# Kernel tuning notes

Measured on AMD Instinct MI355X. Metric: run time of the kernel, lower is better.

Reference implementation:

```python
import jax, jax.numpy as jnp
import numpy as np

B, S, E = 2, 2048, 2048
NQ, NKV, HD = 16, 4, 128
WINDOW = 512
ROPE_BASE = 10000.0


def _rope(x):
    # x: [B, H, S, HD], interleaved even/odd rotation
    half = HD // 2
    freqs = 1.0 / (ROPE_BASE ** (2.0 * jnp.arange(half, dtype=jnp.float32) / HD))
    pos = jnp.arange(x.shape[2], dtype=jnp.float32)
    ang = pos[:, None] * freqs[None, :]            # [S, HD/2]
    cos = jnp.cos(ang)[None, None].astype(x.dtype)  # [1,1,S,HD/2]
    sin = jnp.sin(ang)[None, None].astype(x.dtype)
    xe = x[..., 0::2]
    xo = x[..., 1::2]
    re = xe * cos - xo * sin
    ro = xe * sin + xo * cos
    return jnp.stack([re, ro], axis=-1).reshape(x.shape)


def setup_inputs() -> dict:
    key = jax.random.key(0)
    ks = jax.random.split(key, 9)
    s_in = 1.0 / np.sqrt(E)
    s_out = 1.0 / np.sqrt(NQ * HD)
    return {
        "x": jax.random.normal(ks[0], (B, S, E), jnp.float32),
        "Wq": jax.random.normal(ks[1], (E, NQ * HD), jnp.float32) * s_in,
        "bq": jax.random.normal(ks[2], (NQ * HD,), jnp.float32) * 0.01,
        "Wk": jax.random.normal(ks[3], (E, NKV * HD), jnp.float32) * s_in,
        "bk": jax.random.normal(ks[4], (NKV * HD,), jnp.float32) * 0.01,
        "Wv": jax.random.normal(ks[5], (E, NKV * HD), jnp.float32) * s_in,
        "bv": jax.random.normal(ks[6], (NKV * HD,), jnp.float32) * 0.01,
        "Wo": jax.random.normal(ks[7], (NQ * HD, E), jnp.float32) * s_out,
        "bo": jax.random.normal(ks[8], (E,), jnp.float32) * 0.01,
    }


def reference(x, Wq, bq, Wk, bk, Wv, bv, Wo, bo):
    b, s, _ = x.shape
    q = (x @ Wq + bq).reshape(b, s, NQ, HD).transpose(0, 2, 1, 3)   # [B,NQ,S,HD]
    k = (x @ Wk + bk).reshape(b, s, NKV, HD).transpose(0, 2, 1, 3)  # [B,NKV,S,HD]
    v = (x @ Wv + bv).reshape(b, s, NKV, HD).transpose(0, 2, 1, 3)
    q = _rope(q)
    k = _rope(k)
    rep = NQ // NKV
    k = jnp.repeat(k, rep, axis=1)  # [B,NQ,S,HD], matches torch repeat pattern
    v = jnp.repeat(v, rep, axis=1)
    scores = jnp.einsum("bhqd,bhkd->bhqk", q, k) / np.sqrt(HD)
    i = jnp.arange(s)[:, None]
    j = jnp.arange(s)[None, :]
    allowed = (j <= i) & ((i - j) <= WINDOW)  # sliding-window causal mask
    scores = jnp.where(allowed[None, None], scores, -jnp.inf)
    weights = jax.nn.softmax(scores, axis=-1)
    out = jnp.einsum("bhqk,bhkd->bhqd", weights, v)
    out = out.transpose(0, 2, 1, 3).reshape(b, s, NQ * HD)
    return out @ Wo + bo
```

## Files before the change

kernel.cpp:

```cpp
#include <hip/hip_runtime.h>
#include <hip/hip_bf16.h>
#include <math.h>

#define BB 2
#define SS 2048
#define EE 2048
#define NQ 16
#define NKV 4
#define HD 128
#define WINDOW 512

typedef __hip_bfloat16 bf16;
typedef short short8 __attribute__((ext_vector_type(8)));
typedef float f32x4 __attribute__((ext_vector_type(4)));

__device__ __forceinline__ float toF(bf16 v) { return __bfloat162float(v); }
__device__ __forceinline__ bf16 toB(float v) { return __float2bfloat16(v); }

__device__ __forceinline__ void gld_lds16(const void* g, void* l) {
    __builtin_amdgcn_global_load_lds(
        (const __attribute__((address_space(1))) void*)g,
        (__attribute__((address_space(3))) void*)l, 16, 0, 0);
}

template <int V> __device__ __forceinline__ void waitvm() {
    if constexpr (V == 8)      asm volatile("s_waitcnt vmcnt(8)" ::: "memory");
    else if constexpr (V == 6) asm volatile("s_waitcnt vmcnt(6)" ::: "memory");
    else if constexpr (V == 5) asm volatile("s_waitcnt vmcnt(5)" ::: "memory");
    else if constexpr (V == 4) asm volatile("s_waitcnt vmcnt(4)" ::: "memory");
    else if constexpr (V == 3) asm volatile("s_waitcnt vmcnt(3)" ::: "memory");
    else                       asm volatile("s_waitcnt vmcnt(0)" ::: "memory");
}
__device__ __forceinline__ void waitlgkm0() {
    asm volatile("s_waitcnt lgkmcnt(0)" ::: "memory");
}

__global__ __launch_bounds__(256) void convert_bf16(const float* __restrict__ in,
                                                    bf16* __restrict__ out, int n) {
    int i = (blockIdx.x * 256 + threadIdx.x) * 4;
    if (i >= n) return;
    const float4 v = *(const float4*)(in + i);
    bf16 o[4] = {toB(v.x), toB(v.y), toB(v.z), toB(v.w)};
    *(uint2*)(out + i) = *(const uint2*)o;
}

__global__ __launch_bounds__(256) void convert_transpose(const float* __restrict__ in,
                                                         bf16* __restrict__ out,
                                                         int K, int N) {
    __shared__ float tile[32][33];
    const int t = threadIdx.x;
    const int tx = t & 31, ty = t >> 5;
    const int n0 = blockIdx.x * 32, k0 = blockIdx.y * 32;
#pragma unroll
    for (int r = 0; r < 4; r++)
        tile[ty + r * 8][tx] = in[(size_t)(k0 + ty + r * 8) * N + n0 + tx];
    __syncthreads();
#pragma unroll
    for (int r = 0; r < 4; r++)
        out[(size_t)(n0 + ty + r * 8) * K + k0 + tx] = toB(tile[tx][ty + r * 8]);
}

__global__ __launch_bounds__(256) void convert_transpose_qkv(
    const float* __restrict__ Wq, const float* __restrict__ Wk,
    const float* __restrict__ Wv, bf16* __restrict__ out) {
    __shared__ float tile[32][33];
    const int t = threadIdx.x;
    const int tx = t & 31, ty = t >> 5;
    const int n0 = blockIdx.x * 32, k0 = blockIdx.y * 32;
    const float* src; int N, nl0;
    if (n0 < 2048)      { src = Wq; N = 2048; nl0 = n0; }
    else if (n0 < 2560) { src = Wk; N = 512;  nl0 = n0 - 2048; }
    else                { src = Wv; N = 512;  nl0 = n0 - 2560; }
#pragma unroll
    for (int r = 0; r < 4; r++)
        tile[ty + r * 8][tx] = src[(size_t)(k0 + ty + r * 8) * N + nl0 + tx];
    __syncthreads();
#pragma unroll
    for (int r = 0; r < 4; r++)
        out[(size_t)(n0 + ty + r * 8) * 2048 + k0 + tx] = toB(tile[tx][ty + r * 8]);
}

template <int MODE, int BM, int BN>
__global__ __launch_bounds__(512, 2) void mfma_gemm_v6(
    const bf16* __restrict__ A, const bf16* __restrict__ BT,
    const float* __restrict__ b0, const float* __restrict__ b1,
    const float* __restrict__ b2,
    float* __restrict__ Yf,
    bf16* __restrict__ Yq, bf16* __restrict__ Yk, bf16* __restrict__ Yv,
    int M, int N, int K) {
    constexpr int NI = BM / 2 / 16;
    constexpr int NJ = BN / 4 / 16;
    constexpr int LA = BM / 64;
    constexpr int LB = BN / 64;
    constexpr int SL = LA + LB;

    __shared__ __align__(16) bf16 As[3][BM * 64];
    __shared__ __align__(16) bf16 Bs[3][BN * 64];

    const int tid = threadIdx.x;
    const int lane = tid & 63;
    const int w = tid >> 6;
    const int wm = w >> 2;
    const int wn = w & 3;

    const int gx = gridDim.x, gy = gridDim.y;
    const int lin = blockIdx.y * gx + blockIdx.x;
    const int xcd = lin & 7;
    const int idx = lin >> 3;
    const int rpx = gy >> 3;
    const int tn = idx / rpx;
    const int tm = xcd * rpx + (idx % rpx);
    const int m0 = tm * BM, n0 = tn * BN;

    const int lr = lane & 15;
    const int lq = lane >> 4;
    const int NT = K >> 6;

    const int srow = tid >> 3;
    const int sslot = tid & 7;

    auto stage = [&](int s) {
        bf16* Ad = &As[s % 3][0];
#pragma unroll
        for (int l = 0; l < LA; l++) {
            const int row = l * 64 + srow;
            const int g = sslot ^ (row & 7);
            gld_lds16(A + (size_t)(m0 + row) * K + s * 64 + g * 8,
                      Ad + l * 4096 + w * 512);
        }
        bf16* Bd = &Bs[s % 3][0];
#pragma unroll
        for (int l = 0; l < LB; l++) {
            const int row = l * 64 + srow;
            const int g = sslot ^ (row & 7);
            gld_lds16(BT + (size_t)(n0 + row) * K + s * 64 + g * 8,
                      Bd + l * 4096 + w * 512);
        }
    };

    auto readf = [&](int s, int kk, short8 (&fA)[NI], short8 (&fB)[NJ]) {
        const bf16* Asl = &As[s % 3][0];
        const bf16* Bsl = &Bs[s % 3][0];
#pragma unroll
        for (int i = 0; i < NI; i++) {
            const int row = wm * (NI * 16) + i * 16 + lr;
            const int sl = ((kk << 2) | lq) ^ (row & 7);
            fA[i] = *(const short8*)(Asl + row * 64 + sl * 8);
        }
#pragma unroll
        for (int j = 0; j < NJ; j++) {
            const int row = wn * (NJ * 16) + j * 16 + lr;
            const int sl = ((kk << 2) | lq) ^ (row & 7);
            fB[j] = *(const short8*)(Bsl + row * 64 + sl * 8);
        }
    };

    f32x4 acc[NI][NJ];
#pragma unroll
    for (int i = 0; i < NI; i++)
#pragma unroll
        for (int j = 0; j < NJ; j++) acc[i][j] = (f32x4)0.f;

    auto cluster = [&](short8 (&fA)[NI], short8 (&fB)[NJ]) {
        __builtin_amdgcn_s_setprio(1);
#pragma unroll
        for (int i = 0; i < NI; i++)
#pragma unroll
            for (int j = 0; j < NJ; j++)
                acc[i][j] = __builtin_amdgcn_mfma_f32_16x16x32_bf16(fA[i], fB[j],
                                                                    acc[i][j], 0, 0, 0);
        __builtin_amdgcn_s_setprio(0);
    };

    stage(0); stage(1);
    waitvm<SL>();
    __builtin_amdgcn_s_barrier();
    __builtin_amdgcn_sched_barrier(0);
    short8 fA0[NI], fB0[NJ], fA1[NI], fB1[NJ];
    readf(0, 0, fA0, fB0);

    for (int t = 0; t < NT; ++t) {
        if (t + 2 < NT) stage(t + 2);
        readf(t, 1, fA1, fB1);
        cluster(fA0, fB0);
        waitlgkm0();
        if (t + 2 < NT) waitvm<SL>(); else waitvm<0>();
        __builtin_amdgcn_s_barrier();
        __builtin_amdgcn_sched_barrier(0);
        if (t + 1 < NT) readf(t + 1, 0, fA0, fB0);
        cluster(fA1, fB1);
    }

    if (MODE == 0) {
#pragma unroll
        for (int j = 0; j < NJ; j++) {
            const int col = n0 + wn * (NJ * 16) + j * 16 + lr;
            const float bj = b0[col];
#pragma unroll
            for (int i = 0; i < NI; i++) {
                const int row = m0 + wm * (NI * 16) + i * 16 + lq * 4;
#pragma unroll
                for (int r = 0; r < 4; r++)
                    Yf[(size_t)(row + r) * N + col] = acc[i][j][r] + bj;
            }
        }
    } else {
#pragma unroll
        for (int j = 0; j < NJ; j++) {
            const int gcol = n0 + wn * (NJ * 16) + j * 16 + lr;
            if (gcol < 2560) {
                bf16* outp; const float* bias; int ldc, col;
                if (gcol < 2048) { outp = Yq; bias = b0; ldc = 2048; col = gcol; }
                else             { outp = Yk; bias = b1; ldc = 512;  col = gcol - 2048; }
                const float bj = bias[col];
                const int d2 = (col & 127) >> 1;
                const bool odd = col & 1;
                const float freq = __expf(-0.14384103622589045f * (float)d2);
#pragma unroll
                for (int i = 0; i < NI; i++) {
                    const int row = m0 + wm * (NI * 16) + i * 16 + lq * 4;
#pragma unroll
                    for (int r = 0; r < 4; r++) {
                        const float v = acc[i][j][r] + bj;
                        const float p = __shfl_xor(v, 1, 64);
                        const float ang = (float)((row + r) & (SS - 1)) * freq;
                        float sn, cs;
                        __sincosf(ang, &sn, &cs);
                        const float o = odd ? (p * sn + v * cs) : (v * cs - p * sn);
                        outp[(size_t)(row + r) * ldc + col] = toB(o);
                    }
                }
            } else {
                const int col = gcol - 2560;
                const float bj = b2[col];
                const int hkv = col >> 7, d = col & 127;
#pragma unroll
                for (int i = 0; i < NI; i++) {
                    const int row = m0 + wm * (NI * 16) + i * 16 + lq * 4;
                    const int bb = row >> 11, sr = row & (SS - 1);
                    union { bf16 b[4]; uint2 u; } o4;
#pragma unroll
                    for (int r = 0; r < 4; r++) o4.b[r] = toB(acc[i][j][r] + bj);
                    *(uint2*)(Yv + (((size_t)bb * NKV + hkv) * HD + d) * SS + sr) = o4.u;
                }
            }
        }
    }
}

__global__ __launch_bounds__(256) void attn_mfma(const bf16* __restrict__ Q,
                                                 const bf16* __restrict__ K,
                                                 const bf16* __restrict__ VT,
                                                 bf16* __restrict__ Oout) {
    __shared__ bf16 Ks[64 * 128];
    __shared__ bf16 Vs[128 * 64];
    __shared__ bf16 Ps[4 * 16 * 72];

    const int t = threadIdx.x;
    const int lane = t & 63;
    const int w = t >> 6;
    const int q0 = blockIdx.x * 64;
    const int h = blockIdx.y;
    const int b = blockIdx.z;
    const int hkv = h >> 2;
    const int lr = lane & 15;
    const int lq = lane >> 4;
    const float scale = 0.08838834764831845f;

    short8 aq[4];
    {
        const int q = q0 + w * 16 + lr;
        const bf16* qp = Q + (((size_t)b * SS + q) * NQ + h) * HD + lq * 8;
#pragma unroll
        for (int ks = 0; ks < 4; ks++) aq[ks] = *(const short8*)(qp + ks * 32);
    }

    const int krow = w * 16 + (lane >> 4);
    const int vrow = w * 32 + (lane >> 3);
    const bf16* Kbase = K + ((size_t)b * SS * NKV + hkv) * HD;
    const bf16* Vbase = VT + (((size_t)b * NKV + hkv) * HD) * SS;

    f32x4 Oa[8];
#pragma unroll
    for (int nb = 0; nb < 8; nb++) Oa[nb] = (f32x4)0.f;
    float mprev[4] = {-3.0e38f, -3.0e38f, -3.0e38f, -3.0e38f};
    float lsum[4] = {0.f, 0.f, 0.f, 0.f};

    bf16* Pw = Ps + w * 16 * 72;
    const int jstart = (q0 >= WINDOW) ? (q0 - WINDOW) : 0;

    for (int c0 = jstart; c0 <= q0; c0 += 64) {
        __syncthreads();
#pragma unroll
        for (int s = 0; s < 4; s++) {
            const int r_ = krow + s * 4;
            const int g_ = (lane & 15) ^ (r_ & 7);
            gld_lds16(Kbase + (size_t)(c0 + r_) * (NKV * HD) + g_ * 8,
                      Ks + (w * 16 + s * 4) * 128);
        }
#pragma unroll
        for (int s = 0; s < 4; s++) {
            const int d_ = vrow + s * 8;
            const int g_ = (lane & 7) ^ (d_ & 7);
            gld_lds16(Vbase + (size_t)d_ * SS + c0 + g_ * 8,
                      Vs + (w * 32 + s * 8) * 64);
        }
        __syncthreads();

        f32x4 sa[4];
#pragma unroll
        for (int nb = 0; nb < 4; nb++) sa[nb] = (f32x4)0.f;
#pragma unroll
        for (int ks = 0; ks < 4; ks++) {
#pragma unroll
            for (int nb = 0; nb < 4; nb++) {
                const int slot = (ks * 4 + lq) ^ (lr & 7);
                short8 bk = *(const short8*)(Ks + (nb * 16 + lr) * 128 + slot * 8);
                sa[nb] = __builtin_amdgcn_mfma_f32_16x16x32_bf16(aq[ks], bk, sa[nb], 0, 0, 0);
            }
        }

        const int rowb = q0 + w * 16 + lq * 4;
        const bool noMask = (c0 + 63 <= q0 + w * 16) &&
                            (q0 + w * 16 + 15 - c0 <= WINDOW);
        float pr[4][4], alpha[4];
#pragma unroll
        for (int r = 0; r < 4; r++) {
            const int row = rowb + r;
            float sv[4];
            float mx = -3.0e38f;
            if (noMask) {
#pragma unroll
                for (int nb = 0; nb < 4; nb++) {
                    const float s = sa[nb][r] * scale;
                    sv[nb] = s;
                    mx = fmaxf(mx, s);
                }
            } else {
#pragma unroll
                for (int nb = 0; nb < 4; nb++) {
                    const int col = c0 + nb * 16 + lr;
                    const bool valid = (col <= row) && (row - col <= WINDOW);
                    const float s = valid ? sa[nb][r] * scale : -3.0e38f;
                    sv[nb] = s;
                    mx = fmaxf(mx, s);
                }
            }
#pragma unroll
            for (int off = 1; off < 16; off <<= 1) mx = fmaxf(mx, __shfl_xor(mx, off, 64));
            const float mn = fmaxf(fmaxf(mprev[r], mx), -1.0e30f);
            alpha[r] = __expf(mprev[r] - mn);
            mprev[r] = mn;
            float rs = 0.f;
#pragma unroll
            for (int nb = 0; nb < 4; nb++) {
                const float p = __expf(sv[nb] - mn);
                pr[r][nb] = p;
                rs += p;
            }
#pragma unroll
            for (int off = 1; off < 16; off <<= 1) rs += __shfl_xor(rs, off, 64);
            lsum[r] = lsum[r] * alpha[r] + rs;
        }

#pragma unroll
        for (int r = 0; r < 4; r++)
#pragma unroll
            for (int nb = 0; nb < 4; nb++)
                Pw[(lq * 4 + r) * 72 + nb * 16 + lr] = toB(pr[r][nb]);

#pragma unroll
        for (int nb = 0; nb < 8; nb++)
#pragma unroll
            for (int r = 0; r < 4; r++) Oa[nb][r] *= alpha[r];
#pragma unroll
        for (int ks = 0; ks < 2; ks++) {
            short8 pa = *(const short8*)(Pw + lr * 72 + ks * 32 + lq * 8);
#pragma unroll
            for (int nb = 0; nb < 8; nb++) {
                const int slot = (ks * 4 + lq) ^ (lr & 7);
                short8 bv = *(const short8*)(Vs + (nb * 16 + lr) * 64 + slot * 8);
                Oa[nb] = __builtin_amdgcn_mfma_f32_16x16x32_bf16(pa, bv, Oa[nb], 0, 0, 0);
            }
        }
    }

    float linv[4];
#pragma unroll
    for (int r = 0; r < 4; r++) linv[r] = 1.f / lsum[r];
    const int rowb = q0 + w * 16 + lq * 4;
#pragma unroll
    for (int nb = 0; nb < 8; nb++)
#pragma unroll
        for (int r = 0; r < 4; r++)
            Oout[(((size_t)b * SS + rowb + r) * NQ + h) * HD + nb * 16 + lr] =
                toB(Oa[nb][r] * linv[r]);
}

extern "C" void kernel_launch(void* const* d_in, const int* in_sizes, int n_in,
                              void* d_out, int out_size, void* d_ws, size_t ws_size,
                              hipStream_t stream) {
    const float* x  = (const float*)d_in[0];
    const float* Wq = (const float*)d_in[1];
    const float* bq = (const float*)d_in[2];
    const float* Wk = (const float*)d_in[3];
    const float* bk = (const float*)d_in[4];
    const float* Wv = (const float*)d_in[5];
    const float* bv = (const float*)d_in[6];
    const float* Wo = (const float*)d_in[7];
    const float* bo = (const float*)d_in[8];
    float* out = (float*)d_out;

    const int M   = BB * SS;
    const int DQ  = NQ * HD;
    const int DKV = NKV * HD;
    const int NPK = DQ + 2 * DKV;

    bf16* xb     = (bf16*)d_ws;
    bf16* WqkvT  = xb + (size_t)M * EE;
    bf16* WoT    = WqkvT + (size_t)NPK * EE;
    bf16* Qb     = WoT + (size_t)EE * DQ;
    bf16* Kb     = Qb + (size_t)M * DQ;
    bf16* Vb     = Kb + (size_t)M * DKV;

    convert_bf16<<<(M * EE / 4 + 255) / 256, 256, 0, stream>>>(x, xb, M * EE);
    convert_transpose_qkv<<<dim3(NPK / 32, EE / 32), 256, 0, stream>>>(Wq, Wk, Wv, WqkvT);
    convert_transpose<<<dim3(DQ / 32, DQ / 32), 256, 0, stream>>>(Wo, WoT, DQ, EE);

    mfma_gemm_v6<1, 128, 192><<<dim3(NPK / 192, M / 128), 512, 0, stream>>>(
        xb, WqkvT, bq, bk, bv, nullptr, Qb, Kb, Vb, M, NPK, EE);

    attn_mfma<<<dim3(SS / 64, NQ, BB), 256, 0, stream>>>(Qb, Kb, Vb, Qb);

    mfma_gemm_v6<0, 128, 256><<<dim3(EE / 256, M / 128), 512, 0, stream>>>(
        Qb, WoT, bo, nullptr, nullptr, out, nullptr, nullptr, nullptr, M, EE, DQ);
}
```

Measured before the change: 312.6 us.

## Switch GEMMs to 128x128 tiles with 32x32 MFMA and double-buffer attention K/V

The GEMM kernel moves from 512-thread 128x192/256 tiles using 16x16x32 MFMA to 256-thread 128x128 tiles with K-step 32, using 32x32x16 MFMA and a new swizzle and epilogue mapping. The attention kernel now double-buffers K/V in LDS so the next chunk loads while the current one is computed, with a single barrier per iteration. The intent is more register reuse per MFMA and better occupancy in the GEMMs, plus hiding global load latency in attention. The cost is more LDS in attention and a smaller K-step per GEMM iteration, which means more barriers per iteration.

```diff
diff --git a/kernel.cpp b/kernel.cpp
--- a/kernel.cpp
+++ b/kernel.cpp
@@ -13,6 +13,7 @@
 typedef __hip_bfloat16 bf16;
 typedef short short8 __attribute__((ext_vector_type(8)));
 typedef float f32x4 __attribute__((ext_vector_type(4)));
+typedef float f32x16 __attribute__((ext_vector_type(16)));
 
 __device__ __forceinline__ float toF(bf16 v) { return __bfloat162float(v); }
 __device__ __forceinline__ bf16 toB(float v) { return __float2bfloat16(v); }
@@ -26,7 +27,6 @@
 template <int V> __device__ __forceinline__ void waitvm() {
     if constexpr (V == 8)      asm volatile("s_waitcnt vmcnt(8)" ::: "memory");
     else if constexpr (V == 6) asm volatile("s_waitcnt vmcnt(6)" ::: "memory");
-    else if constexpr (V == 5) asm volatile("s_waitcnt vmcnt(5)" ::: "memory");
     else if constexpr (V == 4) asm volatile("s_waitcnt vmcnt(4)" ::: "memory");
     else if constexpr (V == 3) asm volatile("s_waitcnt vmcnt(3)" ::: "memory");
     else                       asm volatile("s_waitcnt vmcnt(0)" ::: "memory");
@@ -80,28 +80,24 @@
         out[(size_t)(n0 + ty + r * 8) * 2048 + k0 + tx] = toB(tile[tx][ty + r * 8]);
 }
 
-template <int MODE, int BM, int BN>
-__global__ __launch_bounds__(512, 2) void mfma_gemm_v6(
+template <int MODE>
+__global__ __launch_bounds__(256, 3) void mfma_gemm_v7(
     const bf16* __restrict__ A, const bf16* __restrict__ BT,
     const float* __restrict__ b0, const float* __restrict__ b1,
     const float* __restrict__ b2,
     float* __restrict__ Yf,
     bf16* __restrict__ Yq, bf16* __restrict__ Yk, bf16* __restrict__ Yv,
     int M, int N, int K) {
-    constexpr int NI = BM / 2 / 16;
-    constexpr int NJ = BN / 4 / 16;
-    constexpr int LA = BM / 64;
-    constexpr int LB = BN / 64;
-    constexpr int SL = LA + LB;
-
-    __shared__ __align__(16) bf16 As[3][BM * 64];
-    __shared__ __align__(16) bf16 Bs[3][BN * 64];
+    constexpr int SL = 4;
+
+    __shared__ __align__(16) bf16 As[3][128 * 32];
+    __shared__ __align__(16) bf16 Bs[3][128 * 32];
 
     const int tid = threadIdx.x;
     const int lane = tid & 63;
     const int w = tid >> 6;
-    const int wm = w >> 2;
-    const int wn = w & 3;
+    const int wm = w >> 1;
+    const int wn = w & 1;
 
     const int gx = gridDim.x, gy = gridDim.y;
     const int lin = blockIdx.y * gx + blockIdx.x;
@@ -110,64 +106,61 @@
     const int rpx = gy >> 3;
     const int tn = idx / rpx;
     const int tm = xcd * rpx + (idx % rpx);
-    const int m0 = tm * BM, n0 = tn * BN;
-
-    const int lr = lane & 15;
-    const int lq = lane >> 4;
-    const int NT = K >> 6;
-
-    const int srow = tid >> 3;
-    const int sslot = tid & 7;
+    const int m0 = tm * 128, n0 = tn * 128;
+
+    const int l31 = lane & 31;
+    const int l5  = lane >> 5;
+    const int NT = K >> 5;
 
     auto stage = [&](int s) {
         bf16* Ad = &As[s % 3][0];
 #pragma unroll
-        for (int l = 0; l < LA; l++) {
-            const int row = l * 64 + srow;
-            const int g = sslot ^ (row & 7);
-            gld_lds16(A + (size_t)(m0 + row) * K + s * 64 + g * 8,
-                      Ad + l * 4096 + w * 512);
+        for (int l = 0; l < 2; l++) {
+            const int c = w * 2 + l;
+            const int row = c * 16 + (lane >> 2);
+            const int g = (lane & 3) ^ ((row >> 1) & 3);
+            gld_lds16(A + (size_t)(m0 + row) * K + s * 32 + g * 8, Ad + c * 512);
         }
         bf16* Bd = &Bs[s % 3][0];
 #pragma unroll
-        for (int l = 0; l < LB; l++) {
-            const int row = l * 64 + srow;
-            const int g = sslot ^ (row & 7);
-            gld_lds16(BT + (size_t)(n0 + row) * K + s * 64 + g * 8,
-                      Bd + l * 4096 + w * 512);
+        for (int l = 0; l < 2; l++) {
+            const int c = w * 2 + l;
+            const int row = c * 16 + (lane >> 2);
+            const int g = (lane & 3) ^ ((row >> 1) & 3);
+            gld_lds16(BT + (size_t)(n0 + row) * K + s * 32 + g * 8, Bd + c * 512);
         }
     };
 
-    auto readf = [&](int s, int kk, short8 (&fA)[NI], short8 (&fB)[NJ]) {
+    auto readf = [&](int s, int ks, short8 (&fA)[2], short8 (&fB)[2]) {
         const bf16* Asl = &As[s % 3][0];
         const bf16* Bsl = &Bs[s % 3][0];
 #pragma unroll
-        for (int i = 0; i < NI; i++) {
-            const int row = wm * (NI * 16) + i * 16 + lr;
-            const int sl = ((kk << 2) | lq) ^ (row & 7);
-            fA[i] = *(const short8*)(Asl + row * 64 + sl * 8);
-        }
-#pragma unroll
-        for (int j = 0; j < NJ; j++) {
-            const int row = wn * (NJ * 16) + j * 16 + lr;
-            const int sl = ((kk << 2) | lq) ^ (row & 7);
-            fB[j] = *(const short8*)(Bsl + row * 64 + sl * 8);
+        for (int i = 0; i < 2; i++) {
+            const int row = wm * 64 + i * 32 + l31;
+            const int sl = (ks * 2 + l5) ^ ((row >> 1) & 3);
+            fA[i] = *(const short8*)(Asl + row * 32 + sl * 8);
+        }
+#pragma unroll
+        for (int j = 0; j < 2; j++) {
+            const int row = wn * 64 + j * 32 + l31;
+            const int sl = (ks * 2 + l5) ^ ((row >> 1) & 3);
+            fB[j] = *(const short8*)(Bsl + row * 32 + sl * 8);
         }
     };
 
-    f32x4 acc[NI][NJ];
-#pragma unroll
-    for (int i = 0; i < NI; i++)
-#pragma unroll
-        for (int j = 0; j < NJ; j++) acc[i][j] = (f32x4)0.f;
-
-    auto cluster = [&](short8 (&fA)[NI], short8 (&fB)[NJ]) {
+    f32x16 acc[2][2];
+#pragma unroll
+    for (int i = 0; i < 2; i++)
+#pragma unroll
+        for (int j = 0; j < 2; j++) acc[i][j] = (f32x16)0.f;
+
+    auto cluster = [&](short8 (&fA)[2], short8 (&fB)[2]) {
         __builtin_amdgcn_s_setprio(1);
 #pragma unroll
-        for (int i = 0; i < NI; i++)
-#pragma unroll
-            for (int j = 0; j < NJ; j++)
-                acc[i][j] = __builtin_amdgcn_mfma_f32_16x16x32_bf16(fA[i], fB[j],
+        for (int i = 0; i < 2; i++)
+#pragma unroll
+            for (int j = 0; j < 2; j++)
+                acc[i][j] = __builtin_amdgcn_mfma_f32_32x32x16_bf16(fA[i], fB[j],
                                                                     acc[i][j], 0, 0, 0);
         __builtin_amdgcn_s_setprio(0);
     };
@@ -176,7 +169,7 @@
     waitvm<SL>();
     __builtin_amdgcn_s_barrier();
     __builtin_amdgcn_sched_barrier(0);
-    short8 fA0[NI], fB0[NJ], fA1[NI], fB1[NJ];
+    short8 fA0[2], fB0[2], fA1[2], fB1[2];
     readf(0, 0, fA0, fB0);
 
     for (int t = 0; t < NT; ++t) {
@@ -193,21 +186,23 @@
 
     if (MODE == 0) {
 #pragma unroll
-        for (int j = 0; j < NJ; j++) {
-            const int col = n0 + wn * (NJ * 16) + j * 16 + lr;
+        for (int j = 0; j < 2; j++) {
+            const int col = n0 + wn * 64 + j * 32 + l31;
             const float bj = b0[col];
 #pragma unroll
-            for (int i = 0; i < NI; i++) {
-                const int row = m0 + wm * (NI * 16) + i * 16 + lq * 4;
-#pragma unroll
-                for (int r = 0; r < 4; r++)
-                    Yf[(size_t)(row + r) * N + col] = acc[i][j][r] + bj;
+            for (int i = 0; i < 2; i++) {
+                const int rb = m0 + wm * 64 + i * 32 + 4 * l5;
+#pragma unroll
+                for (int reg = 0; reg < 16; reg++) {
+                    const int row = rb + (reg & 3) + 8 * (reg >> 2);
+                    Yf[(size_t)row * N + col] = acc[i][j][reg] + bj;
+                }
             }
         }
     } else {
 #pragma unroll
-        for (int j = 0; j < NJ; j++) {
-            const int gcol = n0 + wn * (NJ * 16) + j * 16 + lr;
+        for (int j = 0; j < 2; j++) {
+            const int gcol = n0 + wn * 64 + j * 32 + l31;
             if (gcol < 2560) {
                 bf16* outp; const float* bias; int ldc, col;
                 if (gcol < 2048) { outp = Yq; bias = b0; ldc = 2048; col = gcol; }
@@ -217,17 +212,18 @@
                 const bool odd = col & 1;
                 const float freq = __expf(-0.14384103622589045f * (float)d2);
 #pragma unroll
-                for (int i = 0; i < NI; i++) {
-                    const int row = m0 + wm * (NI * 16) + i * 16 + lq * 4;
-#pragma unroll
-                    for (int r = 0; r < 4; r++) {
-                        const float v = acc[i][j][r] + bj;
+                for (int i = 0; i < 2; i++) {
+                    const int rb = m0 + wm * 64 + i * 32 + 4 * l5;
+#pragma unroll
+                    for (int reg = 0; reg < 16; reg++) {
+                        const int row = rb + (reg & 3) + 8 * (reg >> 2);
+                        const float v = acc[i][j][reg] + bj;
                         const float p = __shfl_xor(v, 1, 64);
-                        const float ang = (float)((row + r) & (SS - 1)) * freq;
+                        const float ang = (float)(row & (SS - 1)) * freq;
                         float sn, cs;
                         __sincosf(ang, &sn, &cs);
                         const float o = odd ? (p * sn + v * cs) : (v * cs - p * sn);
-                        outp[(size_t)(row + r) * ldc + col] = toB(o);
+                        outp[(size_t)row * ldc + col] = toB(o);
                     }
                 }
             } else {
@@ -235,13 +231,17 @@
                 const float bj = b2[col];
                 const int hkv = col >> 7, d = col & 127;
 #pragma unroll
-                for (int i = 0; i < NI; i++) {
-                    const int row = m0 + wm * (NI * 16) + i * 16 + lq * 4;
-                    const int bb = row >> 11, sr = row & (SS - 1);
-                    union { bf16 b[4]; uint2 u; } o4;
-#pragma unroll
-                    for (int r = 0; r < 4; r++) o4.b[r] = toB(acc[i][j][r] + bj);
-                    *(uint2*)(Yv + (((size_t)bb * NKV + hkv) * HD + d) * SS + sr) = o4.u;
+                for (int i = 0; i < 2; i++) {
+                    const int rb = m0 + wm * 64 + i * 32 + 4 * l5;
+#pragma unroll
+                    for (int rg = 0; rg < 4; rg++) {
+                        const int row = rb + 8 * rg;
+                        const int bb = row >> 11, sr = row & (SS - 1);
+                        union { bf16 b[4]; uint2 u; } o4;
+#pragma unroll
+                        for (int r = 0; r < 4; r++) o4.b[r] = toB(acc[i][j][rg * 4 + r] + bj);
+                        *(uint2*)(Yv + (((size_t)bb * NKV + hkv) * HD + d) * SS + sr) = o4.u;
+                    }
                 }
             }
         }
@@ -252,8 +252,8 @@
                                                  const bf16* __restrict__ K,
                                                  const bf16* __restrict__ VT,
                                                  bf16* __restrict__ Oout) {
-    __shared__ bf16 Ks[64 * 128];
-    __shared__ bf16 Vs[128 * 64];
+    __shared__ bf16 Ks[2][64 * 128];
+    __shared__ bf16 Vs[2][128 * 64];
     __shared__ bf16 Ps[4 * 16 * 72];
 
     const int t = threadIdx.x;
@@ -280,6 +280,25 @@
     const bf16* Kbase = K + ((size_t)b * SS * NKV + hkv) * HD;
     const bf16* Vbase = VT + (((size_t)b * NKV + hkv) * HD) * SS;
 
+    auto stageKV = [&](int c0s, int bufi) {
+        bf16* Kd = &Ks[bufi][0];
+        bf16* Vd = &Vs[bufi][0];
+#pragma unroll
+        for (int s = 0; s < 4; s++) {
+            const int r_ = krow + s * 4;
+            const int g_ = (lane & 15) ^ (r_ & 7);
+            gld_lds16(Kbase + (size_t)(c0s + r_) * (NKV * HD) + g_ * 8,
+                      Kd + (w * 16 + s * 4) * 128);
+        }
+#pragma unroll
+        for (int s = 0; s < 4; s++) {
+            const int d_ = vrow + s * 8;
+            const int g_ = (lane & 7) ^ (d_ & 7);
+            gld_lds16(Vbase + (size_t)d_ * SS + c0s + g_ * 8,
+                      Vd + (w * 32 + s * 8) * 64);
+        }
+    };
+
     f32x4 Oa[8];
 #pragma unroll
     for (int nb = 0; nb < 8; nb++) Oa[nb] = (f32x4)0.f;
@@ -289,23 +308,15 @@
     bf16* Pw = Ps + w * 16 * 72;
     const int jstart = (q0 >= WINDOW) ? (q0 - WINDOW) : 0;
 
+    stageKV(jstart, 0);
+    asm volatile("s_waitcnt vmcnt(0)" ::: "memory");
+    __syncthreads();
+
+    int cb = 0;
     for (int c0 = jstart; c0 <= q0; c0 += 64) {
-        __syncthreads();
-#pragma unroll
-        for (int s = 0; s < 4; s++) {
-            const int r_ = krow + s * 4;
-            const int g_ = (lane & 15) ^ (r_ & 7);
-            gld_lds16(Kbase + (size_t)(c0 + r_) * (NKV * HD) + g_ * 8,
-                      Ks + (w * 16 + s * 4) * 128);
-        }
-#pragma unroll
-        for (int s = 0; s < 4; s++) {
-            const int d_ = vrow + s * 8;
-            const int g_ = (lane & 7) ^ (d_ & 7);
-            gld_lds16(Vbase + (size_t)d_ * SS + c0 + g_ * 8,
-                      Vs + (w * 32 + s * 8) * 64);
-        }
-        __syncthreads();
+        if (c0 + 64 <= q0) stageKV(c0 + 64, cb ^ 1);
+        const bf16* Ksb = &Ks[cb][0];
+        const bf16* Vsb = &Vs[cb][0];
 
         f32x4 sa[4];
 #pragma unroll
@@ -315,7 +326,7 @@
 #pragma unroll
             for (int nb = 0; nb < 4; nb++) {
                 const int slot = (ks * 4 + lq) ^ (lr & 7);
-                short8 bk = *(const short8*)(Ks + (nb * 16 + lr) * 128 + slot * 8);
+                short8 bk = *(const short8*)(Ksb + (nb * 16 + lr) * 128 + slot * 8);
                 sa[nb] = __builtin_amdgcn_mfma_f32_16x16x32_bf16(aq[ks], bk, sa[nb], 0, 0, 0);
             }
         }
@@ -379,10 +390,13 @@
 #pragma unroll
             for (int nb = 0; nb < 8; nb++) {
                 const int slot = (ks * 4 + lq) ^ (lr & 7);
-                short8 bv = *(const short8*)(Vs + (nb * 16 + lr) * 64 + slot * 8);
+                short8 bv = *(const short8*)(Vsb + (nb * 16 + lr) * 64 + slot * 8);
                 Oa[nb] = __builtin_amdgcn_mfma_f32_16x16x32_bf16(pa, bv, Oa[nb], 0, 0, 0);
             }
         }
+
+        __syncthreads();
+        cb ^= 1;
     }
 
     float linv[4];
@@ -427,11 +441,11 @@
     convert_transpose_qkv<<<dim3(NPK / 32, EE / 32), 256, 0, stream>>>(Wq, Wk, Wv, WqkvT);
     convert_transpose<<<dim3(DQ / 32, DQ / 32), 256, 0, stream>>>(Wo, WoT, DQ, EE);
 
-    mfma_gemm_v6<1, 128, 192><<<dim3(NPK / 192, M / 128), 512, 0, stream>>>(
+    mfma_gemm_v7<1><<<dim3(NPK / 128, M / 128), 256, 0, stream>>>(
         xb, WqkvT, bq, bk, bv, nullptr, Qb, Kb, Vb, M, NPK, EE);
 
     attn_mfma<<<dim3(SS / 64, NQ, BB), 256, 0, stream>>>(Qb, Kb, Vb, Qb);
 
-    mfma_gemm_v6<0, 128, 256><<<dim3(EE / 256, M / 128), 512, 0, stream>>>(
+    mfma_gemm_v7<0><<<dim3(EE / 128, M / 128), 256, 0, stream>>>(
         Qb, WoT, bo, nullptr, nullptr, out, nullptr, nullptr, nullptr, M, EE, DQ);
 }
```

Result: no change. 309.6 us (-1.0%).

## Rework GEMM into 256-row tiles with split-K LDS staging and double-buffer attention KV

Applied to the files above, without the earlier changes.

The GEMM kernel moves to 256-row M tiles with a new LDS layout: each 64-wide K step is split into two 32-wide halves, double-buffered, with a new swizzle and barrier-interleaved prefetch between MFMA clusters. Tile shapes and grids for both projection GEMMs change. The attention kernel gains double-buffered K/V LDS tiles so the next chunk is prefetched while the current one is computed. The aim is to hide global-load latency and raise per-block reuse. The cost is more LDS per block, more barriers per iteration and fewer blocks in the grid, which may lower occupancy and wave balance.

```diff
diff --git a/kernel.cpp b/kernel.cpp
--- a/kernel.cpp
+++ b/kernel.cpp
@@ -24,15 +24,10 @@
 }
 
 template <int V> __device__ __forceinline__ void waitvm() {
-    if constexpr (V == 8)      asm volatile("s_waitcnt vmcnt(8)" ::: "memory");
-    else if constexpr (V == 6) asm volatile("s_waitcnt vmcnt(6)" ::: "memory");
-    else if constexpr (V == 5) asm volatile("s_waitcnt vmcnt(5)" ::: "memory");
+    if constexpr (V == 6)      asm volatile("s_waitcnt vmcnt(6)" ::: "memory");
     else if constexpr (V == 4) asm volatile("s_waitcnt vmcnt(4)" ::: "memory");
     else if constexpr (V == 3) asm volatile("s_waitcnt vmcnt(3)" ::: "memory");
     else                       asm volatile("s_waitcnt vmcnt(0)" ::: "memory");
-}
-__device__ __forceinline__ void waitlgkm0() {
-    asm volatile("s_waitcnt lgkmcnt(0)" ::: "memory");
 }
 
 __global__ __launch_bounds__(256) void convert_bf16(const float* __restrict__ in,
@@ -80,22 +75,22 @@
         out[(size_t)(n0 + ty + r * 8) * 2048 + k0 + tx] = toB(tile[tx][ty + r * 8]);
 }
 
-template <int MODE, int BM, int BN>
-__global__ __launch_bounds__(512, 2) void mfma_gemm_v6(
+template <int MODE, int BN>
+__global__ __launch_bounds__(512, 2) void mfma_gemm_v8(
     const bf16* __restrict__ A, const bf16* __restrict__ BT,
     const float* __restrict__ b0, const float* __restrict__ b1,
     const float* __restrict__ b2,
     float* __restrict__ Yf,
     bf16* __restrict__ Yq, bf16* __restrict__ Yk, bf16* __restrict__ Yv,
     int M, int N, int K) {
-    constexpr int NI = BM / 2 / 16;
-    constexpr int NJ = BN / 4 / 16;
-    constexpr int LA = BM / 64;
-    constexpr int LB = BN / 64;
-    constexpr int SL = LA + LB;
-
-    __shared__ __align__(16) bf16 As[3][BM * 64];
-    __shared__ __align__(16) bf16 Bs[3][BN * 64];
+    constexpr int NI = 8;
+    constexpr int NJ = BN / 64;
+    constexpr int LA = 2;
+    constexpr int LB = BN / 128;
+    constexpr int KEEP = LA + LB;
+
+    __shared__ __align__(16) bf16 As[2][2][256 * 32];
+    __shared__ __align__(16) bf16 Bs[2][2][BN * 32];
 
     const int tid = threadIdx.x;
     const int lane = tid & 63;
@@ -110,48 +105,47 @@
     const int rpx = gy >> 3;
     const int tn = idx / rpx;
     const int tm = xcd * rpx + (idx % rpx);
-    const int m0 = tm * BM, n0 = tn * BN;
+    const int m0 = tm * 256, n0 = tn * BN;
 
     const int lr = lane & 15;
     const int lq = lane >> 4;
     const int NT = K >> 6;
 
-    const int srow = tid >> 3;
-    const int sslot = tid & 7;
-
-    auto stage = [&](int s) {
-        bf16* Ad = &As[s % 3][0];
+    auto stA = [&](int b, int kh, int t) {
 #pragma unroll
         for (int l = 0; l < LA; l++) {
-            const int row = l * 64 + srow;
-            const int g = sslot ^ (row & 7);
-            gld_lds16(A + (size_t)(m0 + row) * K + s * 64 + g * 8,
-                      Ad + l * 4096 + w * 512);
-        }
-        bf16* Bd = &Bs[s % 3][0];
+            const int g16 = w * LA + l;
+            const int row = g16 * 16 + (lane >> 2);
+            const int kg = (lane & 3) ^ ((row >> 1) & 3);
+            gld_lds16(A + (size_t)(m0 + row) * K + t * 64 + kh * 32 + kg * 8,
+                      &As[b][kh][g16 * 512]);
+        }
+    };
+    auto stB = [&](int b, int kh, int t) {
 #pragma unroll
         for (int l = 0; l < LB; l++) {
-            const int row = l * 64 + srow;
-            const int g = sslot ^ (row & 7);
-            gld_lds16(BT + (size_t)(n0 + row) * K + s * 64 + g * 8,
-                      Bd + l * 4096 + w * 512);
-        }
-    };
-
-    auto readf = [&](int s, int kk, short8 (&fA)[NI], short8 (&fB)[NJ]) {
-        const bf16* Asl = &As[s % 3][0];
-        const bf16* Bsl = &Bs[s % 3][0];
-#pragma unroll
-        for (int i = 0; i < NI; i++) {
-            const int row = wm * (NI * 16) + i * 16 + lr;
-            const int sl = ((kk << 2) | lq) ^ (row & 7);
-            fA[i] = *(const short8*)(Asl + row * 64 + sl * 8);
-        }
+            const int g16 = w * LB + l;
+            const int row = g16 * 16 + (lane >> 2);
+            const int kg = (lane & 3) ^ ((row >> 1) & 3);
+            gld_lds16(BT + (size_t)(n0 + row) * K + t * 64 + kh * 32 + kg * 8,
+                      &Bs[b][kh][g16 * 512]);
+        }
+    };
+
+    auto rdA = [&](int b, int kh, int i0, short8 (&af)[4]) {
+#pragma unroll
+        for (int i2 = 0; i2 < 4; i2++) {
+            const int row = wm * 128 + (i0 + i2) * 16 + lr;
+            const int sl = lq ^ ((row >> 1) & 3);
+            af[i2] = *(const short8*)(&As[b][kh][row * 32 + sl * 8]);
+        }
+    };
+    auto rdB = [&](int b, int kh, short8 (&bf)[NJ]) {
 #pragma unroll
         for (int j = 0; j < NJ; j++) {
             const int row = wn * (NJ * 16) + j * 16 + lr;
-            const int sl = ((kk << 2) | lq) ^ (row & 7);
-            fB[j] = *(const short8*)(Bsl + row * 64 + sl * 8);
+            const int sl = lq ^ ((row >> 1) & 3);
+            bf[j] = *(const short8*)(&Bs[b][kh][row * 32 + sl * 8]);
         }
     };
 
@@ -161,34 +155,51 @@
 #pragma unroll
         for (int j = 0; j < NJ; j++) acc[i][j] = (f32x4)0.f;
 
-    auto cluster = [&](short8 (&fA)[NI], short8 (&fB)[NJ]) {
+    auto cl = [&](int i0, short8 (&af)[4], short8 (&bf)[NJ]) {
         __builtin_amdgcn_s_setprio(1);
 #pragma unroll
-        for (int i = 0; i < NI; i++)
+        for (int i2 = 0; i2 < 4; i2++)
 #pragma unroll
             for (int j = 0; j < NJ; j++)
-                acc[i][j] = __builtin_amdgcn_mfma_f32_16x16x32_bf16(fA[i], fB[j],
-                                                                    acc[i][j], 0, 0, 0);
+                acc[i0 + i2][j] = __builtin_amdgcn_mfma_f32_16x16x32_bf16(
+                    af[i2], bf[j], acc[i0 + i2][j], 0, 0, 0);
         __builtin_amdgcn_s_setprio(0);
     };
 
-    stage(0); stage(1);
-    waitvm<SL>();
+    stA(0, 0, 0); stB(0, 0, 0); stA(0, 1, 0); stB(0, 1, 0);
+    waitvm<0>();
     __builtin_amdgcn_s_barrier();
-    __builtin_amdgcn_sched_barrier(0);
-    short8 fA0[NI], fB0[NJ], fA1[NI], fB1[NJ];
-    readf(0, 0, fA0, fB0);
-
+
+    short8 afr[4], bfr[NJ];
     for (int t = 0; t < NT; ++t) {
-        if (t + 2 < NT) stage(t + 2);
-        readf(t, 1, fA1, fB1);
-        cluster(fA0, fB0);
-        waitlgkm0();
-        if (t + 2 < NT) waitvm<SL>(); else waitvm<0>();
-        __builtin_amdgcn_s_barrier();
+        const int cb = t & 1;
+        const bool st = (t + 1 < NT);
+        rdB(cb, 0, bfr);
+        rdA(cb, 0, 0, afr);
+        if (st) stA(cb ^ 1, 0, t + 1);
+        __builtin_amdgcn_s_barrier();
+        cl(0, afr, bfr);
+        __builtin_amdgcn_s_barrier();
+        rdA(cb, 0, 4, afr);
+        if (st) stB(cb ^ 1, 0, t + 1);
+        __builtin_amdgcn_s_barrier();
+        cl(4, afr, bfr);
+        if (st) waitvm<KEEP>(); else waitvm<0>();
         __builtin_amdgcn_sched_barrier(0);
-        if (t + 1 < NT) readf(t + 1, 0, fA0, fB0);
-        cluster(fA1, fB1);
+        __builtin_amdgcn_s_barrier();
+        rdB(cb, 1, bfr);
+        rdA(cb, 1, 0, afr);
+        if (st) stA(cb ^ 1, 1, t + 1);
+        __builtin_amdgcn_s_barrier();
+        cl(0, afr, bfr);
+        __builtin_amdgcn_s_barrier();
+        rdA(cb, 1, 4, afr);
+        if (st) stB(cb ^ 1, 1, t + 1);
+        __builtin_amdgcn_s_barrier();
+        cl(4, afr, bfr);
+        if (st) waitvm<KEEP>(); else waitvm<0>();
+        __builtin_amdgcn_sched_barrier(0);
+        __builtin_amdgcn_s_barrier();
     }
 
     if (MODE == 0) {
@@ -198,7 +209,7 @@
             const float bj = b0[col];
 #pragma unroll
             for (int i = 0; i < NI; i++) {
-                const int row = m0 + wm * (NI * 16) + i * 16 + lq * 4;
+                const int row = m0 + wm * 128 + i * 16 + lq * 4;
 #pragma unroll
                 for (int r = 0; r < 4; r++)
                     Yf[(size_t)(row + r) * N + col] = acc[i][j][r] + bj;
@@ -218,7 +229,7 @@
                 const float freq = __expf(-0.14384103622589045f * (float)d2);
 #pragma unroll
                 for (int i = 0; i < NI; i++) {
-                    const int row = m0 + wm * (NI * 16) + i * 16 + lq * 4;
+                    const int row = m0 + wm * 128 + i * 16 + lq * 4;
 #pragma unroll
                     for (int r = 0; r < 4; r++) {
                         const float v = acc[i][j][r] + bj;
@@ -236,7 +247,7 @@
                 const int hkv = col >> 7, d = col & 127;
 #pragma unroll
                 for (int i = 0; i < NI; i++) {
-                    const int row = m0 + wm * (NI * 16) + i * 16 + lq * 4;
+                    const int row = m0 + wm * 128 + i * 16 + lq * 4;
                     const int bb = row >> 11, sr = row & (SS - 1);
                     union { bf16 b[4]; uint2 u; } o4;
 #pragma unroll
@@ -252,8 +263,8 @@
                                                  const bf16* __restrict__ K,
                                                  const bf16* __restrict__ VT,
                                                  bf16* __restrict__ Oout) {
-    __shared__ bf16 Ks[64 * 128];
-    __shared__ bf16 Vs[128 * 64];
+    __shared__ bf16 Ks[2][64 * 128];
+    __shared__ bf16 Vs[2][128 * 64];
     __shared__ bf16 Ps[4 * 16 * 72];
 
     const int t = threadIdx.x;
@@ -280,6 +291,25 @@
     const bf16* Kbase = K + ((size_t)b * SS * NKV + hkv) * HD;
     const bf16* Vbase = VT + (((size_t)b * NKV + hkv) * HD) * SS;
 
+    auto stageKV = [&](int c0s, int bufi) {
+        bf16* Kd = &Ks[bufi][0];
+        bf16* Vd = &Vs[bufi][0];
+#pragma unroll
+        for (int s = 0; s < 4; s++) {
+            const int r_ = krow + s * 4;
+            const int g_ = (lane & 15) ^ (r_ & 7);
+            gld_lds16(Kbase + (size_t)(c0s + r_) * (NKV * HD) + g_ * 8,
+                      Kd + (w * 16 + s * 4) * 128);
+        }
+#pragma unroll
+        for (int s = 0; s < 4; s++) {
+            const int d_ = vrow + s * 8;
+            const int g_ = (lane & 7) ^ (d_ & 7);
+            gld_lds16(Vbase + (size_t)d_ * SS + c0s + g_ * 8,
+                      Vd + (w * 32 + s * 8) * 64);
+        }
+    };
+
     f32x4 Oa[8];
 #pragma unroll
     for (int nb = 0; nb < 8; nb++) Oa[nb] = (f32x4)0.f;
@@ -289,23 +319,15 @@
     bf16* Pw = Ps + w * 16 * 72;
     const int jstart = (q0 >= WINDOW) ? (q0 - WINDOW) : 0;
 
+    stageKV(jstart, 0);
+    asm volatile("s_waitcnt vmcnt(0)" ::: "memory");
+    __syncthreads();
+
+    int cb = 0;
     for (int c0 = jstart; c0 <= q0; c0 += 64) {
-        __syncthreads();
-#pragma unroll
-        for (int s = 0; s < 4; s++) {
-            const int r_ = krow + s * 4;
-            const int g_ = (lane & 15) ^ (r_ & 7);
-            gld_lds16(Kbase + (size_t)(c0 + r_) * (NKV * HD) + g_ * 8,
-                      Ks + (w * 16 + s * 4) * 128);
-        }
-#pragma unroll
-        for (int s = 0; s < 4; s++) {
-            const int d_ = vrow + s * 8;
-            const int g_ = (lane & 7) ^ (d_ & 7);
-            gld_lds16(Vbase + (size_t)d_ * SS + c0 + g_ * 8,
-                      Vs + (w * 32 + s * 8) * 64);
-        }
-        __syncthreads();
+        if (c0 + 64 <= q0) stageKV(c0 + 64, cb ^ 1);
+        const bf16* Ksb = &Ks[cb][0];
+        const bf16* Vsb = &Vs[cb][0];
 
         f32x4 sa[4];
 #pragma unroll
@@ -315,7 +337,7 @@
 #pragma unroll
             for (int nb = 0; nb < 4; nb++) {
                 const int slot = (ks * 4 + lq) ^ (lr & 7);
-                short8 bk = *(const short8*)(Ks + (nb * 16 + lr) * 128 + slot * 8);
+                short8 bk = *(const short8*)(Ksb + (nb * 16 + lr) * 128 + slot * 8);
                 sa[nb] = __builtin_amdgcn_mfma_f32_16x16x32_bf16(aq[ks], bk, sa[nb], 0, 0, 0);
             }
         }
@@ -379,10 +401,13 @@
 #pragma unroll
             for (int nb = 0; nb < 8; nb++) {
                 const int slot = (ks * 4 + lq) ^ (lr & 7);
-                short8 bv = *(const short8*)(Vs + (nb * 16 + lr) * 64 + slot * 8);
+                short8 bv = *(const short8*)(Vsb + (nb * 16 + lr) * 64 + slot * 8);
                 Oa[nb] = __builtin_amdgcn_mfma_f32_16x16x32_bf16(pa, bv, Oa[nb], 0, 0, 0);
             }
         }
+
+        __syncthreads();
+        cb ^= 1;
     }
 
     float linv[4];
@@ -427,11 +452,11 @@
     convert_transpose_qkv<<<dim3(NPK / 32, EE / 32), 256, 0, stream>>>(Wq, Wk, Wv, WqkvT);
     convert_transpose<<<dim3(DQ / 32, DQ / 32), 256, 0, stream>>>(Wo, WoT, DQ, EE);
 
-    mfma_gemm_v6<1, 128, 192><<<dim3(NPK / 192, M / 128), 512, 0, stream>>>(
+    mfma_gemm_v8<1, 256><<<dim3(NPK / 256, M / 256), 512, 0, stream>>>(
         xb, WqkvT, bq, bk, bv, nullptr, Qb, Kb, Vb, M, NPK, EE);
 
     attn_mfma<<<dim3(SS / 64, NQ, BB), 256, 0, stream>>>(Qb, Kb, Vb, Qb);
 
-    mfma_gemm_v6<0, 128, 256><<<dim3(EE / 256, M / 128), 512, 0, stream>>>(
+    mfma_gemm_v8<0, 128><<<dim3(EE / 128, M / 256), 512, 0, stream>>>(
         Qb, WoT, bo, nullptr, nullptr, out, nullptr, nullptr, nullptr, M, EE, DQ);
 }
```

After: 312.8 us. Within noise of the previous version (+0.0%).
